# Kernel tuning notes

Measured on AMD Instinct MI355X. Metric: run time of the kernel, lower is better.

## Reference

```python
import jax, jax.numpy as jnp
import numpy as np

S, B, D, W = 2048, 4, 1024, 256  # seq_len, batch, d_model, local_window_size


def create_local_mask(seq_len, w):
    # Faithful to source: tril(w-1) then tril(-(w-1)) -> keeps j <= i-(w-1)
    m = jnp.ones((seq_len, seq_len), dtype=bool)
    m = jnp.tril(m, w - 1)
    m = jnp.tril(m, -(w - 1))
    return m


def setup_inputs() -> dict:
    key = jax.random.key(0)
    ks = jax.random.split(key, 12)
    w = lambda k: jax.random.normal(k, (D, D), dtype=jnp.float32) * 0.02
    return {
        "query": jax.random.normal(ks[0], (S, B, D), dtype=jnp.float32),
        "key_in": jax.random.normal(ks[1], (S, B, D), dtype=jnp.float32),
        "value": jax.random.normal(ks[2], (S, B, D), dtype=jnp.float32),
        "Wq": w(ks[3]), "bq": jnp.zeros((D,), jnp.float32),
        "Wk": w(ks[4]), "bk": jnp.zeros((D,), jnp.float32),
        "Wv": w(ks[5]), "bv": jnp.zeros((D,), jnp.float32),
        "pos_bias": jax.random.normal(ks[6], (S, S), dtype=jnp.float32) * 0.02,
        "Wo": w(ks[7]), "bo": jnp.zeros((D,), jnp.float32),
        "mask": jnp.ones((S, S, 1), dtype=bool),
    }


def reference(query, key_in, value, Wq, bq, Wk, bk, Wv, bv, pos_bias, Wo, bo, mask):
    # Linear projections (torch Linear: x @ W.T + b)
    q = jnp.einsum('sbd,ed->sbe', query, Wq) + bq
    k = jnp.einsum('sbd,ed->sbe', key_in, Wk) + bk
    v = jnp.einsum('sbd,ed->sbe', value, Wv) + bv

    local_mask = create_local_mask(S, W)
    pb = (pos_bias * local_mask.astype(pos_bias.dtype))[:, :, None]  # [S,S,1]
    pb = jnp.where(mask, pb, -jnp.inf)

    max_key = jnp.max(k, axis=0, keepdims=True)          # [1,B,D]
    max_pb = jnp.max(pb, axis=1, keepdims=True)          # [S,1,1]
    exp_key = jnp.exp(k - max_key)                       # [S,B,D]
    exp_pb = jnp.exp(pb - max_pb)                        # [S,S,B] after broadcast

    num = jnp.einsum('ijb,jbd->ibd', exp_pb, exp_key * v)
    den = jnp.einsum('ijb,jbd->ibd', exp_pb, exp_key)
    y = jax.nn.sigmoid(q) * num / den
    return jnp.einsum('sbd,ed->sbe', y, Wo) + bo
```

## Files before the change

kernel.cpp:

```cpp
#include <hip/hip_runtime.h>
#include <hip/hip_bf16.h>
#include <cstdint>


typedef short short8 __attribute__((ext_vector_type(8)));
typedef float f32x4 __attribute__((ext_vector_type(4)));

#define S_LEN 2048
#define NBD 4096
#define SBD 8388608
#define DD 1048576
#define SS 4194304

#define ASZ 8192
#define BUFSZ 24576
#define AS1 __attribute__((address_space(1)))
#define AS3 __attribute__((address_space(3)))

__device__ __forceinline__ unsigned short f2bf(float f) {
  union { float f; unsigned int u; } x; x.f = f;
  unsigned int u = x.u;
  unsigned int r = u + 0x7fffu + ((u >> 16) & 1u);
  return (unsigned short)(r >> 16);
}
__device__ __forceinline__ float bf2f(unsigned short b) {
  union { unsigned int u; float f; } x; x.u = ((unsigned int)b) << 16;
  return x.f;
}

__global__ __launch_bounds__(256) void k_cvt3(
    const float* __restrict__ a, const float* __restrict__ b, const float* __restrict__ c,
    unsigned short* __restrict__ oa, unsigned short* __restrict__ ob,
    unsigned short* __restrict__ oc) {
  const int w = blockIdx.x;
  const int arr = w >> 11;
  const int b2 = w & 2047;
  const float* src = arr == 0 ? a : (arr == 1 ? b : c);
  unsigned short* dst = arr == 0 ? oa : (arr == 1 ? ob : oc);
  const size_t t0 = (size_t)b2 * 256 + threadIdx.x;
#pragma unroll
  for (int it = 0; it < 2; ++it) {
    const size_t base = (t0 + (size_t)it * 524288) * 8;
    float4 x0 = *(const float4*)(src + base);
    float4 x1 = *(const float4*)(src + base + 4);
    short8 s;
    s[0] = (short)f2bf(x0.x); s[1] = (short)f2bf(x0.y);
    s[2] = (short)f2bf(x0.z); s[3] = (short)f2bf(x0.w);
    s[4] = (short)f2bf(x1.x); s[5] = (short)f2bf(x1.y);
    s[6] = (short)f2bf(x1.z); s[7] = (short)f2bf(x1.w);
    *(short8*)(dst + base) = s;
  }
}

__global__ void k_cvt4w(const float* __restrict__ wq, const float* __restrict__ wk,
                        const float* __restrict__ wv, const float* __restrict__ wo,
                        unsigned short* __restrict__ wcat, unsigned short* __restrict__ wob) {
  int i = (blockIdx.x * blockDim.x + threadIdx.x) * 4;
  float4 fq = *(const float4*)(wq + i);
  float4 fk = *(const float4*)(wk + i);
  float4 fv = *(const float4*)(wv + i);
  float4 fo = *(const float4*)(wo + i);
  ushort4 u;
  u.x = f2bf(fq.x); u.y = f2bf(fq.y); u.z = f2bf(fq.z); u.w = f2bf(fq.w);
  *(ushort4*)(wcat + i) = u;
  u.x = f2bf(fk.x); u.y = f2bf(fk.y); u.z = f2bf(fk.z); u.w = f2bf(fk.w);
  *(ushort4*)(wcat + DD + i) = u;
  u.x = f2bf(fv.x); u.y = f2bf(fv.y); u.z = f2bf(fv.z); u.w = f2bf(fv.w);
  *(ushort4*)(wcat + 2 * DD + i) = u;
  u.x = f2bf(fo.x); u.y = f2bf(fo.y); u.z = f2bf(fo.z); u.w = f2bf(fo.w);
  *(ushort4*)(wob + i) = u;
}

__global__ void k_build_c(const float* __restrict__ pb, unsigned short* __restrict__ C) {
  int i4 = (blockIdx.x * blockDim.x + threadIdx.x) * 4;
  float4 p = *(const float4*)(pb + i4);
  const int i = i4 >> 11;
  const int j = i4 & 2047;
  ushort4 o;
  o.x = f2bf((i >= j + 255) ? expm1f(p.x) : 0.0f);
  o.y = f2bf((i >= j + 256) ? expm1f(p.y) : 0.0f);
  o.z = f2bf((i >= j + 257) ? expm1f(p.z) : 0.0f);
  o.w = f2bf((i >= j + 258) ? expm1f(p.w) : 0.0f);
  *(ushort4*)(C + i4) = o;
}

__global__ __launch_bounds__(256) void k_eu_transpose(
    const unsigned short* __restrict__ kbf, const unsigned short* __restrict__ vbf,
    unsigned short* __restrict__ Mt, float* __restrict__ totals) {
  __shared__ unsigned short Lu[64][65];
  __shared__ unsigned short Le[64][65];
  const int n0 = blockIdx.x * 64;
  const int j0 = blockIdx.y * 64;
  const int t = threadIdx.x;
  const int c = t & 63;
  const int jq = t >> 6;
  float ptu = 0.f, pte = 0.f;
#pragma unroll 4
  for (int s = 0; s < 16; ++s) {
    int jj = jq + s * 4;
    size_t g = (size_t)(j0 + jj) * NBD + n0 + c;
    float kv = bf2f(kbf[g]);
    float vv = bf2f(vbf[g]);
    float e = __expf(kv);
    float u = e * vv;
    Le[jj][c] = f2bf(e);
    Lu[jj][c] = f2bf(u);
    pte += e; ptu += u;
  }
  atomicAdd(&totals[n0 + c], ptu);
  atomicAdd(&totals[NBD + n0 + c], pte);
  __syncthreads();
  const int jj2 = t & 63;
  const int nq = t >> 6;
#pragma unroll 4
  for (int s = 0; s < 16; ++s) {
    int nn = nq + s * 4;
    int ru = 2 * n0 + 32 * (nn >> 4) + (nn & 15);
    Mt[(size_t)ru * S_LEN + j0 + jj2] = Lu[jj2][nn];
    Mt[(size_t)(ru + 16) * S_LEN + j0 + jj2] = Le[jj2][nn];
  }
}


#define SBAR() do { __builtin_amdgcn_sched_barrier(0); __builtin_amdgcn_s_barrier(); \
                    __builtin_amdgcn_sched_barrier(0); } while (0)
#define VM(n)  do { asm volatile("s_waitcnt vmcnt(" #n ")" ::: "memory"); \
                    __builtin_amdgcn_sched_barrier(0); } while (0)
#define LGK0() do { asm volatile("s_waitcnt lgkmcnt(0)" ::: "memory"); \
                    __builtin_amdgcn_sched_barrier(0); } while (0)

#define STAGE(tile, bidx) do {                                                            \
    const int k0s_ = (tile) * 64;                                                         \
    _Pragma("unroll") for (int q_ = 0; q_ < 2; ++q_) {                                    \
      const int g_ = wave * 2 + q_;                                                       \
      __builtin_amdgcn_global_load_lds(                                                   \
          (const AS1 unsigned int*)(Ag + (size_t)(m0 + g_ * 8 + lr) * LDA + k0s_ + lc),   \
          (AS3 unsigned int*)&lds[(bidx) * BUFSZ + g_ * 512], 16, 0, 0);                  \
    }                                                                                     \
    _Pragma("unroll") for (int q_ = 0; q_ < 4; ++q_) {                                    \
      const int g_ = wave * 4 + q_;                                                       \
      __builtin_amdgcn_global_load_lds(                                                   \
          (const AS1 unsigned int*)(Bg + (size_t)(n0 + g_ * 8 + lr) * LDB + k0s_ + lc),   \
          (AS3 unsigned int*)&lds[(bidx) * BUFSZ + ASZ + g_ * 512], 16, 0, 0);            \
    }                                                                                     \
  } while (0)

#define READF(RA, RB, bidx, ks) do {                                                      \
    const int kof_ = (ks) * 32 + lh8;                                                     \
    _Pragma("unroll") for (int f_ = 0; f_ < 4; ++f_) {                                    \
      const int row_ = wr + f_ * 16 + l15;                                                \
      RA[f_] = *(const short8*)&lds[(bidx) * BUFSZ + row_ * 64 + (kof_ ^ swz)];           \
    }                                                                                     \
    _Pragma("unroll") for (int f_ = 0; f_ < 4; ++f_) {                                    \
      const int row_ = wc + f_ * 16 + l15;                                                \
      RB[f_] = *(const short8*)&lds[(bidx) * BUFSZ + ASZ + row_ * 64 + (kof_ ^ swz)];     \
    }                                                                                     \
  } while (0)

#define MFMA16(RA, RB) do {                                                               \
    __builtin_amdgcn_s_setprio(1);                                                        \
    _Pragma("unroll") for (int i_ = 0; i_ < 4; ++i_)                                      \
    _Pragma("unroll") for (int j_ = 0; j_ < 4; ++j_)                                      \
      acc[i_][j_] = __builtin_amdgcn_mfma_f32_16x16x32_bf16(RA[i_], RB[j_],               \
                                                            acc[i_][j_], 0, 0, 0);       \
    __builtin_amdgcn_s_setprio(0);                                                        \
  } while (0)

template <int MODE>
__global__ __launch_bounds__(512, 2) void k_gemm8(
    const unsigned short* __restrict__ A0, const unsigned short* __restrict__ A1,
    const unsigned short* __restrict__ A2, const unsigned short* __restrict__ Bg,
    const float* __restrict__ x0, const float* __restrict__ x1, const float* __restrict__ x2,
    const unsigned short* __restrict__ sq,
    void* __restrict__ out0, void* __restrict__ out1, void* __restrict__ out2) {
  __shared__ unsigned short lds[3 * BUFSZ];

  const int tid = threadIdx.x;
  const int wave = tid >> 6, lane = tid & 63;
  const int l15 = lane & 15, lh = lane >> 4;
  const int lh8 = lh * 8;
  const int swz = (l15 & 7) * 8;
  const int lr = lane >> 3;
  const int lc = ((lane & 7) ^ lr) * 8;
  const int wr = (wave >> 2) * 64, wc = (wave & 3) * 64;

  const int w = blockIdx.x;
  int mb, nb;
  if (MODE == 0) { const int xcd = w & 7, slot = w >> 3; mb = xcd * 8 + slot / 12; nb = slot % 12; }
  else if (MODE == 1) { mb = 15 - (w >> 5); nb = w & 31; }
  else { const int xcd = w & 7, slot = w >> 3; mb = xcd * 8 + (slot >> 2); nb = slot & 3; }
  const int m0 = mb * 128, n0 = nb * 256;
  const int LDA = (MODE == 1) ? 2048 : 1024;
  const int LDB = (MODE == 1) ? 2048 : 1024;
  const int NT = (MODE == 1) ? (mb > 0 ? 2 * mb - 1 : 0) : 16;
  const int grp = (MODE == 0) ? (nb >> 2) : 0;
  const unsigned short* Ag = (MODE == 0) ? (grp == 0 ? A0 : (grp == 1 ? A1 : A2)) : A0;

  f32x4 acc[4][4];
#pragma unroll
  for (int i = 0; i < 4; ++i)
#pragma unroll
    for (int j = 0; j < 4; ++j)
      acc[i][j] = (f32x4){0.f, 0.f, 0.f, 0.f};

  short8 ra0[4], rb0[4], ra1[4], rb1[4];

  if (NT > 0) {
    STAGE(0, 0);
    if (NT > 1) STAGE(1, 1);
    if (NT > 2) STAGE(2, 2);
    if (NT > 2) VM(12); else if (NT > 1) VM(6); else VM(0);
    SBAR();
    READF(ra0, rb0, 0, 0);
    int cb = 0;
    for (int t = 0; t < NT; ++t) {
      READF(ra1, rb1, cb, 1);
      MFMA16(ra0, rb0);
      if (t < NT - 1) {
        LGK0();
        if (t + 2 <= NT - 1) VM(6); else VM(0);
        SBAR();
        int nbuf = cb + 1; if (nbuf == 3) nbuf = 0;
        READF(ra0, rb0, nbuf, 0);
        if (t + 3 <= NT - 1) STAGE(t + 3, cb);
        cb = nbuf;
        MFMA16(ra1, rb1);
      } else {
        MFMA16(ra1, rb1);
      }
    }
  }

  if (MODE == 0) {
    const float* bias = grp == 0 ? x0 : (grp == 1 ? x1 : x2);
    unsigned short* outp = (unsigned short*)(grp == 0 ? out0 : (grp == 1 ? out1 : out2));
#pragma unroll
    for (int i = 0; i < 4; ++i)
#pragma unroll
      for (int j = 0; j < 4; ++j)
#pragma unroll
        for (int r = 0; r < 4; ++r) {
          const int row = m0 + wr + i * 16 + lh * 4 + r;
          const int col = (n0 + wc + j * 16 + l15) & 1023;
          float v = acc[i][j][r] + bias[col];
          if (grp == 0) v = 1.0f / (1.0f + __expf(-v));
          outp[(size_t)row * 1024 + col] = f2bf(v);
        }
  } else if (MODE == 1) {
    unsigned short* Y = (unsigned short*)out0;
#pragma unroll
    for (int i = 0; i < 4; ++i)
#pragma unroll
      for (int p = 0; p < 2; ++p) {
        const int n = ((n0 + wc) >> 1) + 16 * p + l15;
        const float tu = x0[n];
        const float te = x0[NBD + n];
#pragma unroll
        for (int r = 0; r < 4; ++r) {
          const int row = m0 + wr + i * 16 + lh * 4 + r;
          const size_t idx = (size_t)row * NBD + n;
          const float num = tu + acc[i][2 * p][r];
          const float den = te + acc[i][2 * p + 1][r];
          Y[idx] = f2bf(bf2f(sq[idx]) * num / den);
        }
      }
  } else {
    float* outp = (float*)out0;
#pragma unroll
    for (int i = 0; i < 4; ++i)
#pragma unroll
      for (int j = 0; j < 4; ++j)
#pragma unroll
        for (int r = 0; r < 4; ++r) {
          const int row = m0 + wr + i * 16 + lh * 4 + r;
          const int col = n0 + wc + j * 16 + l15;
          outp[(size_t)row * 1024 + col] = acc[i][j][r] + x0[col];
        }
  }
}

extern "C" void kernel_launch(void* const* d_in, const int* in_sizes, int n_in,
                              void* d_out, int out_size, void* d_ws, size_t ws_size,
                              hipStream_t stream) {
  const float* query   = (const float*)d_in[0];
  const float* key_in  = (const float*)d_in[1];
  const float* value   = (const float*)d_in[2];
  const float* Wq      = (const float*)d_in[3];
  const float* bq      = (const float*)d_in[4];
  const float* Wk      = (const float*)d_in[5];
  const float* bk      = (const float*)d_in[6];
  const float* Wv      = (const float*)d_in[7];
  const float* bv      = (const float*)d_in[8];
  const float* pos_bias= (const float*)d_in[9];
  const float* Wo      = (const float*)d_in[10];
  const float* bo      = (const float*)d_in[11];
  float* out = (float*)d_out;

  char* wp = (char*)d_ws;
  auto alloc = [&](size_t bytes) -> char* {
    char* p = wp;
    wp += (bytes + 255) & ~(size_t)255;
    return p;
  };
  unsigned short* Xq   = (unsigned short*)alloc((size_t)SBD * 2);
  unsigned short* Xk   = (unsigned short*)alloc((size_t)SBD * 2);
  unsigned short* Xv   = (unsigned short*)alloc((size_t)SBD * 2);
  unsigned short* Wcat = (unsigned short*)alloc((size_t)3 * DD * 2);
  unsigned short* Wob  = (unsigned short*)alloc((size_t)DD * 2);
  unsigned short* Cb   = (unsigned short*)alloc((size_t)SS * 2);
  unsigned short* sigq = (unsigned short*)alloc((size_t)SBD * 2);
  unsigned short* kbf  = (unsigned short*)alloc((size_t)SBD * 2);
  unsigned short* vbf  = (unsigned short*)alloc((size_t)SBD * 2);
  unsigned short* Mt   = (unsigned short*)alloc((size_t)8192 * S_LEN * 2);
  float*          tot  = (float*)alloc((size_t)8192 * 4);
  unsigned short* Yb   = (unsigned short*)alloc((size_t)SBD * 2);

  k_cvt3<<<6144, 256, 0, stream>>>(query, key_in, value, Xq, Xk, Xv);
  k_cvt4w<<<DD / 4 / 256, 256, 0, stream>>>(Wq, Wk, Wv, Wo, Wcat, Wob);

  k_build_c<<<SS / 4 / 256, 256, 0, stream>>>(pos_bias, Cb);

  k_gemm8<0><<<768, 512, 0, stream>>>(Xq, Xk, Xv, Wcat, bq, bk, bv, nullptr,
                                      sigq, kbf, vbf);

  hipMemsetAsync(tot, 0, 8192 * sizeof(float), stream);
  dim3 ge(NBD / 64, S_LEN / 64);
  k_eu_transpose<<<ge, 256, 0, stream>>>(kbf, vbf, Mt, tot);

  k_gemm8<1><<<512, 512, 0, stream>>>(Cb, nullptr, nullptr, Mt, tot, nullptr, nullptr,
                                      sigq, Yb, nullptr, nullptr);

  k_gemm8<2><<<256, 512, 0, stream>>>(Yb, nullptr, nullptr, Wob, bo, nullptr, nullptr,
                                      nullptr, out, nullptr, nullptr);
}
```

Before: 177.4 us.

## Use K=32 tiled GEMM with higher occupancy for projection and attention GEMMs

Adds a new GEMM kernel that stages 32-wide K tiles, using half the LDS per buffer and a single register fragment set, with launch bounds asking for 4 blocks per CU instead of 2. It is used for the QKV projection and the local-attention GEMM. The attention GEMM's block order is also interleaved so that heavy and light row blocks alternate, to balance the triangular work. The output projection moves to a specialised copy of the old kernel. The goal is more concurrent waves to hide memory latency, at the cost of twice as many barriers per K and no LDS swizzle, which risks bank conflicts.

```diff
diff --git a/kernel.cpp b/kernel.cpp
--- a/kernel.cpp
+++ b/kernel.cpp
@@ -14,6 +14,8 @@
 
 #define ASZ 8192
 #define BUFSZ 24576
+#define GASZ 4096
+#define GBUF 12288
 #define AS1 __attribute__((address_space(1)))
 #define AS3 __attribute__((address_space(3)))
 
@@ -121,7 +123,6 @@
   }
 }
 
-
 #define SBAR() do { __builtin_amdgcn_sched_barrier(0); __builtin_amdgcn_s_barrier(); \
                     __builtin_amdgcn_sched_barrier(0); } while (0)
 #define VM(n)  do { asm volatile("s_waitcnt vmcnt(" #n ")" ::: "memory"); \
@@ -129,18 +130,142 @@
 #define LGK0() do { asm volatile("s_waitcnt lgkmcnt(0)" ::: "memory"); \
                     __builtin_amdgcn_sched_barrier(0); } while (0)
 
+
+#define G32_STAGE(tile, bidx) do {                                                        \
+    const int k0_ = (tile) * 32;                                                          \
+    __builtin_amdgcn_global_load_lds(                                                     \
+        (const AS1 unsigned int*)(Ag + (size_t)(m0 + wave * 16 + lr4) * LDA + k0_ + lc4), \
+        (AS3 unsigned int*)&lds[(bidx) * GBUF + wave * 512 + lane * 8], 16, 0, 0);        \
+    _Pragma("unroll") for (int q_ = 0; q_ < 2; ++q_) {                                    \
+      const int g_ = wave * 2 + q_;                                                       \
+      __builtin_amdgcn_global_load_lds(                                                   \
+          (const AS1 unsigned int*)(Bg + (size_t)(n0 + g_ * 16 + lr4) * LDB + k0_ + lc4), \
+          (AS3 unsigned int*)&lds[(bidx) * GBUF + GASZ + g_ * 512 + lane * 8], 16, 0, 0); \
+    }                                                                                     \
+  } while (0)
+
+#define G32_READF(RA, RB, bidx) do {                                                      \
+    _Pragma("unroll") for (int f_ = 0; f_ < 4; ++f_)                                      \
+      RA[f_] = *(const short8*)&lds[(bidx) * GBUF + (wr + f_ * 16 + l15) * 32 + lh8];     \
+    _Pragma("unroll") for (int f_ = 0; f_ < 4; ++f_)                                      \
+      RB[f_] = *(const short8*)&lds[(bidx) * GBUF + GASZ + (wc + f_ * 16 + l15) * 32 + lh8];\
+  } while (0)
+
+#define G32_MFMA(RA, RB) do {                                                             \
+    __builtin_amdgcn_s_setprio(1);                                                        \
+    _Pragma("unroll") for (int i_ = 0; i_ < 4; ++i_)                                      \
+    _Pragma("unroll") for (int j_ = 0; j_ < 4; ++j_)                                      \
+      acc[i_][j_] = __builtin_amdgcn_mfma_f32_16x16x32_bf16(RA[i_], RB[j_],               \
+                                                            acc[i_][j_], 0, 0, 0);       \
+    __builtin_amdgcn_s_setprio(0);                                                        \
+  } while (0)
+
+template <int MODE>
+__global__ __launch_bounds__(512, 4) void k_g32(
+    const unsigned short* __restrict__ A0, const unsigned short* __restrict__ A1,
+    const unsigned short* __restrict__ A2, const unsigned short* __restrict__ Bg,
+    const float* __restrict__ x0, const float* __restrict__ x1, const float* __restrict__ x2,
+    const unsigned short* __restrict__ sq,
+    void* __restrict__ out0, void* __restrict__ out1, void* __restrict__ out2) {
+  __shared__ unsigned short lds[3 * GBUF];
+
+  const int tid = threadIdx.x;
+  const int wave = tid >> 6, lane = tid & 63;
+  const int l15 = lane & 15, lh = lane >> 4;
+  const int lh8 = lh * 8;
+  const int lr4 = lane >> 2;
+  const int lc4 = (lane & 3) * 8;
+  const int wr = (wave >> 2) * 64, wc = (wave & 3) * 64;
+
+  const int w = blockIdx.x;
+  int mb, nb;
+  if (MODE == 0) { const int xcd = w & 7, slot = w >> 3; mb = xcd * 8 + slot / 12; nb = slot % 12; }
+  else { const int q = w >> 5; mb = q < 8 ? 15 - q : q - 8; nb = w & 31; }
+  const int m0 = mb * 128, n0 = nb * 256;
+  const int LDA = (MODE == 1) ? 2048 : 1024;
+  const int LDB = (MODE == 1) ? 2048 : 1024;
+  const int NT = (MODE == 1) ? (mb > 0 ? 4 * mb - 3 : 0) : 32;
+  const int grp = (MODE == 0) ? (nb >> 2) : 0;
+  const unsigned short* Ag = (MODE == 0) ? (grp == 0 ? A0 : (grp == 1 ? A1 : A2)) : A0;
+
+  f32x4 acc[4][4];
+#pragma unroll
+  for (int i = 0; i < 4; ++i)
+#pragma unroll
+    for (int j = 0; j < 4; ++j)
+      acc[i][j] = (f32x4){0.f, 0.f, 0.f, 0.f};
+
+  short8 ra[4], rb[4];
+
+  if (NT > 0) {
+    G32_STAGE(0, 0);
+    if (NT > 1) G32_STAGE(1, 1);
+    if (NT > 2) G32_STAGE(2, 2);
+    if (NT > 2) VM(6); else if (NT > 1) VM(3); else VM(0);
+    SBAR();
+    G32_READF(ra, rb, 0);
+    int cb = 0;
+    for (int t = 0; t < NT; ++t) {
+      G32_MFMA(ra, rb);
+      if (t == NT - 1) break;
+      LGK0();
+      if (t + 2 <= NT - 1) VM(3); else VM(0);
+      SBAR();
+      int nbuf = cb + 1; if (nbuf == 3) nbuf = 0;
+      G32_READF(ra, rb, nbuf);
+      if (t + 3 <= NT - 1) G32_STAGE(t + 3, cb);
+      cb = nbuf;
+    }
+  }
+
+  if (MODE == 0) {
+    const float* bias = grp == 0 ? x0 : (grp == 1 ? x1 : x2);
+    unsigned short* outp = (unsigned short*)(grp == 0 ? out0 : (grp == 1 ? out1 : out2));
+#pragma unroll
+    for (int i = 0; i < 4; ++i)
+#pragma unroll
+      for (int j = 0; j < 4; ++j)
+#pragma unroll
+        for (int r = 0; r < 4; ++r) {
+          const int row = m0 + wr + i * 16 + lh * 4 + r;
+          const int col = (n0 + wc + j * 16 + l15) & 1023;
+          float v = acc[i][j][r] + bias[col];
+          if (grp == 0) v = 1.0f / (1.0f + __expf(-v));
+          outp[(size_t)row * 1024 + col] = f2bf(v);
+        }
+  } else {
+    unsigned short* Y = (unsigned short*)out0;
+#pragma unroll
+    for (int i = 0; i < 4; ++i)
+#pragma unroll
+      for (int p = 0; p < 2; ++p) {
+        const int n = ((n0 + wc) >> 1) + 16 * p + l15;
+        const float tu = x0[n];
+        const float te = x0[NBD + n];
+#pragma unroll
+        for (int r = 0; r < 4; ++r) {
+          const int row = m0 + wr + i * 16 + lh * 4 + r;
+          const size_t idx = (size_t)row * NBD + n;
+          const float num = tu + acc[i][2 * p][r];
+          const float den = te + acc[i][2 * p + 1][r];
+          Y[idx] = f2bf(bf2f(sq[idx]) * num / den);
+        }
+      }
+  }
+}
+
 #define STAGE(tile, bidx) do {                                                            \
     const int k0s_ = (tile) * 64;                                                         \
     _Pragma("unroll") for (int q_ = 0; q_ < 2; ++q_) {                                    \
       const int g_ = wave * 2 + q_;                                                       \
       __builtin_amdgcn_global_load_lds(                                                   \
-          (const AS1 unsigned int*)(Ag + (size_t)(m0 + g_ * 8 + lr) * LDA + k0s_ + lc),   \
+          (const AS1 unsigned int*)(Ag + (size_t)(m0 + g_ * 8 + lr) * 1024 + k0s_ + lc),  \
           (AS3 unsigned int*)&lds[(bidx) * BUFSZ + g_ * 512], 16, 0, 0);                  \
     }                                                                                     \
     _Pragma("unroll") for (int q_ = 0; q_ < 4; ++q_) {                                    \
       const int g_ = wave * 4 + q_;                                                       \
       __builtin_amdgcn_global_load_lds(                                                   \
-          (const AS1 unsigned int*)(Bg + (size_t)(n0 + g_ * 8 + lr) * LDB + k0s_ + lc),   \
+          (const AS1 unsigned int*)(Bg + (size_t)(n0 + g_ * 8 + lr) * 1024 + k0s_ + lc),  \
           (AS3 unsigned int*)&lds[(bidx) * BUFSZ + ASZ + g_ * 512], 16, 0, 0);            \
     }                                                                                     \
   } while (0)
@@ -157,22 +282,9 @@
     }                                                                                     \
   } while (0)
 
-#define MFMA16(RA, RB) do {                                                               \
-    __builtin_amdgcn_s_setprio(1);                                                        \
-    _Pragma("unroll") for (int i_ = 0; i_ < 4; ++i_)                                      \
-    _Pragma("unroll") for (int j_ = 0; j_ < 4; ++j_)                                      \
-      acc[i_][j_] = __builtin_amdgcn_mfma_f32_16x16x32_bf16(RA[i_], RB[j_],               \
-                                                            acc[i_][j_], 0, 0, 0);       \
-    __builtin_amdgcn_s_setprio(0);                                                        \
-  } while (0)
-
-template <int MODE>
-__global__ __launch_bounds__(512, 2) void k_gemm8(
-    const unsigned short* __restrict__ A0, const unsigned short* __restrict__ A1,
-    const unsigned short* __restrict__ A2, const unsigned short* __restrict__ Bg,
-    const float* __restrict__ x0, const float* __restrict__ x1, const float* __restrict__ x2,
-    const unsigned short* __restrict__ sq,
-    void* __restrict__ out0, void* __restrict__ out1, void* __restrict__ out2) {
+__global__ __launch_bounds__(512, 2) void k_gout(
+    const unsigned short* __restrict__ Ag0, const unsigned short* __restrict__ Bg,
+    const float* __restrict__ bias, float* __restrict__ outp) {
   __shared__ unsigned short lds[3 * BUFSZ];
 
   const int tid = threadIdx.x;
@@ -185,16 +297,10 @@
   const int wr = (wave >> 2) * 64, wc = (wave & 3) * 64;
 
   const int w = blockIdx.x;
-  int mb, nb;
-  if (MODE == 0) { const int xcd = w & 7, slot = w >> 3; mb = xcd * 8 + slot / 12; nb = slot % 12; }
-  else if (MODE == 1) { mb = 15 - (w >> 5); nb = w & 31; }
-  else { const int xcd = w & 7, slot = w >> 3; mb = xcd * 8 + (slot >> 2); nb = slot & 3; }
+  const int xcd = w & 7, slot = w >> 3;
+  const int mb = xcd * 8 + (slot >> 2), nb = slot & 3;
   const int m0 = mb * 128, n0 = nb * 256;
-  const int LDA = (MODE == 1) ? 2048 : 1024;
-  const int LDB = (MODE == 1) ? 2048 : 1024;
-  const int NT = (MODE == 1) ? (mb > 0 ? 2 * mb - 1 : 0) : 16;
-  const int grp = (MODE == 0) ? (nb >> 2) : 0;
-  const unsigned short* Ag = (MODE == 0) ? (grp == 0 ? A0 : (grp == 1 ? A1 : A2)) : A0;
+  const unsigned short* Ag = Ag0;
 
   f32x4 acc[4][4];
 #pragma unroll
@@ -205,78 +311,49 @@
 
   short8 ra0[4], rb0[4], ra1[4], rb1[4];
 
-  if (NT > 0) {
-    STAGE(0, 0);
-    if (NT > 1) STAGE(1, 1);
-    if (NT > 2) STAGE(2, 2);
-    if (NT > 2) VM(12); else if (NT > 1) VM(6); else VM(0);
-    SBAR();
-    READF(ra0, rb0, 0, 0);
-    int cb = 0;
-    for (int t = 0; t < NT; ++t) {
-      READF(ra1, rb1, cb, 1);
-      MFMA16(ra0, rb0);
-      if (t < NT - 1) {
-        LGK0();
-        if (t + 2 <= NT - 1) VM(6); else VM(0);
-        SBAR();
-        int nbuf = cb + 1; if (nbuf == 3) nbuf = 0;
-        READF(ra0, rb0, nbuf, 0);
-        if (t + 3 <= NT - 1) STAGE(t + 3, cb);
-        cb = nbuf;
-        MFMA16(ra1, rb1);
-      } else {
-        MFMA16(ra1, rb1);
+  STAGE(0, 0); STAGE(1, 1); STAGE(2, 2);
+  VM(12);
+  SBAR();
+  READF(ra0, rb0, 0, 0);
+  int cb = 0;
+  const int NT = 16;
+  for (int t = 0; t < NT; ++t) {
+    READF(ra1, rb1, cb, 1);
+    __builtin_amdgcn_s_setprio(1);
+#pragma unroll
+    for (int i_ = 0; i_ < 4; ++i_)
+#pragma unroll
+      for (int j_ = 0; j_ < 4; ++j_)
+        acc[i_][j_] = __builtin_amdgcn_mfma_f32_16x16x32_bf16(ra0[i_], rb0[j_], acc[i_][j_], 0, 0, 0);
+    __builtin_amdgcn_s_setprio(0);
+    if (t < NT - 1) {
+      LGK0();
+      if (t + 2 <= NT - 1) VM(6); else VM(0);
+      SBAR();
+      int nbuf = cb + 1; if (nbuf == 3) nbuf = 0;
+      READF(ra0, rb0, nbuf, 0);
+      if (t + 3 <= NT - 1) STAGE(t + 3, cb);
+      cb = nbuf;
+    }
+    __builtin_amdgcn_s_setprio(1);
+#pragma unroll
+    for (int i_ = 0; i_ < 4; ++i_)
+#pragma unroll
+      for (int j_ = 0; j_ < 4; ++j_)
+        acc[i_][j_] = __builtin_amdgcn_mfma_f32_16x16x32_bf16(ra1[i_], rb1[j_], acc[i_][j_], 0, 0, 0);
+    __builtin_amdgcn_s_setprio(0);
+  }
+
+#pragma unroll
+  for (int i = 0; i < 4; ++i)
+#pragma unroll
+    for (int j = 0; j < 4; ++j)
+#pragma unroll
+      for (int r = 0; r < 4; ++r) {
+        const int row = m0 + wr + i * 16 + lh * 4 + r;
+        const int col = n0 + wc + j * 16 + l15;
+        outp[(size_t)row * 1024 + col] = acc[i][j][r] + bias[col];
       }
-    }
-  }
-
-  if (MODE == 0) {
-    const float* bias = grp == 0 ? x0 : (grp == 1 ? x1 : x2);
-    unsigned short* outp = (unsigned short*)(grp == 0 ? out0 : (grp == 1 ? out1 : out2));
-#pragma unroll
-    for (int i = 0; i < 4; ++i)
-#pragma unroll
-      for (int j = 0; j < 4; ++j)
-#pragma unroll
-        for (int r = 0; r < 4; ++r) {
-          const int row = m0 + wr + i * 16 + lh * 4 + r;
-          const int col = (n0 + wc + j * 16 + l15) & 1023;
-          float v = acc[i][j][r] + bias[col];
-          if (grp == 0) v = 1.0f / (1.0f + __expf(-v));
-          outp[(size_t)row * 1024 + col] = f2bf(v);
-        }
-  } else if (MODE == 1) {
-    unsigned short* Y = (unsigned short*)out0;
-#pragma unroll
-    for (int i = 0; i < 4; ++i)
-#pragma unroll
-      for (int p = 0; p < 2; ++p) {
-        const int n = ((n0 + wc) >> 1) + 16 * p + l15;
-        const float tu = x0[n];
-        const float te = x0[NBD + n];
-#pragma unroll
-        for (int r = 0; r < 4; ++r) {
-          const int row = m0 + wr + i * 16 + lh * 4 + r;
-          const size_t idx = (size_t)row * NBD + n;
-          const float num = tu + acc[i][2 * p][r];
-          const float den = te + acc[i][2 * p + 1][r];
-          Y[idx] = f2bf(bf2f(sq[idx]) * num / den);
-        }
-      }
-  } else {
-    float* outp = (float*)out0;
-#pragma unroll
-    for (int i = 0; i < 4; ++i)
-#pragma unroll
-      for (int j = 0; j < 4; ++j)
-#pragma unroll
-        for (int r = 0; r < 4; ++r) {
-          const int row = m0 + wr + i * 16 + lh * 4 + r;
-          const int col = n0 + wc + j * 16 + l15;
-          outp[(size_t)row * 1024 + col] = acc[i][j][r] + x0[col];
-        }
-  }
 }
 
 extern "C" void kernel_launch(void* const* d_in, const int* in_sizes, int n_in,
@@ -320,16 +397,15 @@
 
   k_build_c<<<SS / 4 / 256, 256, 0, stream>>>(pos_bias, Cb);
 
-  k_gemm8<0><<<768, 512, 0, stream>>>(Xq, Xk, Xv, Wcat, bq, bk, bv, nullptr,
-                                      sigq, kbf, vbf);
+  k_g32<0><<<768, 512, 0, stream>>>(Xq, Xk, Xv, Wcat, bq, bk, bv, nullptr,
+                                    sigq, kbf, vbf);
 
   hipMemsetAsync(tot, 0, 8192 * sizeof(float), stream);
   dim3 ge(NBD / 64, S_LEN / 64);
   k_eu_transpose<<<ge, 256, 0, stream>>>(kbf, vbf, Mt, tot);
 
-  k_gemm8<1><<<512, 512, 0, stream>>>(Cb, nullptr, nullptr, Mt, tot, nullptr, nullptr,
-                                      sigq, Yb, nullptr, nullptr);
-
-  k_gemm8<2><<<256, 512, 0, stream>>>(Yb, nullptr, nullptr, Wob, bo, nullptr, nullptr,
-                                      nullptr, out, nullptr, nullptr);
-}
+  k_g32<1><<<512, 512, 0, stream>>>(Cb, nullptr, nullptr, Mt, tot, nullptr, nullptr,
+                                    sigq, Yb, nullptr, nullptr);
+
+  k_gout<<<256, 512, 0, stream>>>(Yb, Wob, bo, out);
+}
```

Result: slower. 185.4 us (+4.5%).
